# Kernel tuning notes

Measured on AMD Instinct MI355X. Metric: run time of the kernel, lower is better.

## Reference

```python
import jax, jax.numpy as jnp
import numpy as np

B, N, K, CLS = 256, 15, 520, 800  # batch, points per streamline, k+k_global, classes
EPS = 1e-5


def _bn(x, g, b, m, v, axis=1):
    # eval-mode BatchNorm with running stats
    shape = [1] * x.ndim
    shape[axis] = -1
    rs = lambda a: a.reshape(shape)
    return rs(g) * (x - rs(m)) * jax.lax.rsqrt(rs(v) + EPS) + rs(b)


def setup_inputs():
    key = jax.random.key(0)
    kit = iter(jax.random.split(key, 24))
    nk = lambda: next(kit)
    p = {}
    p["pts"] = jax.random.normal(nk(), (B, N, 3), jnp.float32)
    p["label"] = jax.random.randint(nk(), (B,), 0, CLS)
    p["info_point_set"] = jax.random.normal(nk(), (B, K, N, 3), jnp.float32)

    def lin(cout, cin):
        w = jax.random.normal(nk(), (cout, cin), jnp.float32) * (1.0 / np.sqrt(cin))
        return w, jnp.zeros((cout,), jnp.float32)

    def bn(c):
        return (jnp.ones((c,), jnp.float32), jnp.zeros((c,), jnp.float32),
                jax.random.normal(nk(), (c,), jnp.float32) * 0.05,
                jnp.ones((c,), jnp.float32))

    p["w_info"], p["b_info"] = lin(64, 6)
    p["g_info"], p["be_info"], p["m_info"], p["v_info"] = bn(64)
    p["w2"], p["b2"] = lin(128, 64)
    p["g2"], p["be2"], p["m2"], p["v2"] = bn(128)
    p["w3"], p["b3"] = lin(1024, 128)
    p["g3"], p["be3"], p["m3"], p["v3"] = bn(1024)
    p["wf1"], p["bf1"] = lin(512, 1024)
    p["gf1"], p["bef1"], p["mf1"], p["vf1"] = bn(512)
    p["wf2"], p["bf2"] = lin(256, 512)
    p["gf2"], p["bef2"], p["mf2"], p["vf2"] = bn(256)
    p["wf3"], p["bf3"] = lin(CLS, 256)
    return p


def reference(pts, label, info_point_set,
              w_info, b_info, g_info, be_info, m_info, v_info,
              w2, b2, g2, be2, m2, v2,
              w3, b3, g3, be3, m3, v3,
              wf1, bf1, gf1, bef1, mf1, vf1,
              wf2, bf2, gf2, bef2, mf2, vf2,
              wf3, bf3):
    x = jnp.transpose(pts, (0, 2, 1))                      # [B,3,N]
    ips = jnp.transpose(info_point_set, (0, 3, 2, 1))      # [B,3,N,K]
    xr = jnp.broadcast_to(x[..., None], ips.shape)         # [B,3,N,K]
    h = jnp.concatenate([ips - xr, xr], axis=1)            # [B,6,N,K]
    h = jnp.einsum('oc,bcnk->bonk', w_info, h) + b_info[None, :, None, None]
    h = jax.nn.relu(_bn(h, g_info, be_info, m_info, v_info))
    h = jnp.max(h, axis=-1)                                # [B,64,N]  (max over neighbors)
    h2 = jax.nn.relu(_bn(jnp.einsum('oc,bcn->bon', w2, h) + b2[None, :, None],
                         g2, be2, m2, v2))                 # [B,128,N]
    h3 = _bn(jnp.einsum('oc,bcn->bon', w3, h2) + b3[None, :, None],
             g3, be3, m3, v3)                              # [B,1024,N]
    g = jnp.max(h3, axis=2)                                # [B,1024] global max-pool
    f1 = jax.nn.relu(_bn(g @ wf1.T + bf1, gf1, bef1, mf1, vf1, axis=1))
    f2 = jax.nn.relu(_bn(f1 @ wf2.T + bf2, gf2, bef2, mf2, vf2, axis=1))  # dropout identity (eval)
    ret = f2 @ wf3.T + bf3                                 # [B,CLS]
    return (ret, f2)
```

## Files before the change

kernel.cpp:

```cpp
#include <hip/hip_runtime.h>
#include <math.h>

#define EPS 1e-5f

typedef __attribute__((ext_vector_type(8))) short short8v;
typedef __attribute__((ext_vector_type(4))) float f32x4;
typedef __attribute__((ext_vector_type(16))) float f32x16;

__device__ __forceinline__ unsigned short bf16r(float x) {
    unsigned u = __float_as_uint(x);
    return (unsigned short)((u + 0x7FFFu + ((u >> 16) & 1u)) >> 16);
}
__device__ __forceinline__ float bf2f(unsigned short h) {
    return __uint_as_float(((unsigned)h) << 16);
}
__device__ __forceinline__ unsigned packhl(float x) {
    const unsigned short h = bf16r(x);
    const unsigned short l = bf16r(x - bf2f(h));
    return (unsigned)h | ((unsigned)l << 16);
}

__global__ __launch_bounds__(256) void k_pre(
    const float* __restrict__ w3, const float* __restrict__ b3,
    const float* __restrict__ g3, const float* __restrict__ be3,
    const float* __restrict__ m3, const float* __restrict__ v3,
    const float* __restrict__ w2, const float* __restrict__ b2,
    const float* __restrict__ g2, const float* __restrict__ be2,
    const float* __restrict__ m2, const float* __restrict__ v2,
    const float* __restrict__ w_info, const float* __restrict__ b_info,
    const float* __restrict__ g_info, const float* __restrict__ be_info,
    const float* __restrict__ m_info, const float* __restrict__ v_info,
    const float* __restrict__ bf1, const float* __restrict__ gf1,
    const float* __restrict__ bef1, const float* __restrict__ mf1,
    const float* __restrict__ vf1,
    const float* __restrict__ bf2, const float* __restrict__ gf2,
    const float* __restrict__ bef2, const float* __restrict__ mf2,
    const float* __restrict__ vf2,
    const float* __restrict__ wf1, const float* __restrict__ wf2,
    const float* __restrict__ wf3,
    unsigned short* __restrict__ Bh, unsigned short* __restrict__ Bl,
    float* __restrict__ bias3,
    float4* __restrict__ w2q, float* __restrict__ bias2,
    unsigned short* __restrict__ Bedge,
    float4* __restrict__ qTab4,
    float* __restrict__ sf1, float* __restrict__ cf1,
    float* __restrict__ sf2, float* __restrict__ cf2,
    unsigned short* __restrict__ B1h, unsigned short* __restrict__ B1l,
    unsigned short* __restrict__ B2h, unsigned short* __restrict__ B2l,
    unsigned short* __restrict__ B3h, unsigned short* __restrict__ B3l)
{
    const int blk = blockIdx.x, tid = threadIdx.x;
    if (blk < 64) {
        const int t = blk * 256 + tid;
        const int kt = t >> 12;
        const int nt = (t >> 6) & 63;
        const int lane = t & 63;
        const int o  = nt * 16 + (lane & 15);
        const int kb = kt * 32 + ((lane >> 4) << 3);
        const float a3 = g3[o] * rsqrtf(v3[o] + EPS);
        #pragma unroll
        for (int j = 0; j < 8; ++j) {
            const float wv = a3 * w3[(size_t)o * 128 + kb + j];
            const unsigned short hi = bf16r(wv);
            Bh[(size_t)t * 8 + j] = hi;
            Bl[(size_t)t * 8 + j] = bf16r(wv - bf2f(hi));
        }
    } else if (blk == 64) {
        for (int idx = tid; idx < 2048; idx += 256) {
            const int o2 = idx & 127, cq = idx >> 7;
            const float a2 = g2[o2] * rsqrtf(v2[o2] + EPS);
            const float4 w = *(const float4*)(w2 + (size_t)o2 * 64 + cq * 4);
            w2q[cq * 128 + o2] = make_float4(a2 * w.x, a2 * w.y, a2 * w.z, a2 * w.w);
        }
        if (tid < 128) {
            const float a2 = g2[tid] * rsqrtf(v2[tid] + EPS);
            bias2[tid] = a2 * (b2[tid] - m2[tid]) + be2[tid];
        }
    } else if (blk == 65) {
        if (tid < 128) {
            const int nt = tid >> 6, lane = tid & 63;
            const int grp = lane >> 5;
            const int o = nt * 32 + (lane & 31);
            const float a = g_info[o] * rsqrtf(v_info[o] + EPS);
            const float c0 = a * w_info[o*6+0];
            const float c1 = a * w_info[o*6+1];
            const float c2 = a * w_info[o*6+2];
            const unsigned short ch0 = bf16r(c0), ch1 = bf16r(c1), ch2 = bf16r(c2);
            const unsigned short cl0 = bf16r(c0 - bf2f(ch0));
            const unsigned short cl1 = bf16r(c1 - bf2f(ch1));
            const unsigned short cl2 = bf16r(c2 - bf2f(ch2));
            unsigned short out[8] = {0,0,0,0,0,0,0,0};
            if (grp == 0) {
                out[0]=ch0; out[1]=ch1; out[2]=ch2;
                out[3]=cl0; out[4]=cl1; out[5]=cl2;
                out[6]=ch0; out[7]=ch1;
            } else {
                out[0]=ch2;
            }
            #pragma unroll
            for (int j = 0; j < 8; ++j)
                Bedge[(size_t)(nt*64 + lane)*8 + j] = out[j];
        }
        if (tid < 64) {
            const int o = tid;
            const float w0 = w_info[o*6+0], w1 = w_info[o*6+1], w2c = w_info[o*6+2];
            const float w3c = w_info[o*6+3], w4 = w_info[o*6+4], w5 = w_info[o*6+5];
            const float a = g_info[o] * rsqrtf(v_info[o] + EPS);
            qTab4[o] = make_float4(a*(w3c-w0), a*(w4-w1), a*(w5-w2c),
                                   a*(b_info[o]-m_info[o]) + be_info[o]);
        }
        for (int c = tid; c < 1024; c += 256) {
            const float a3 = g3[c] * rsqrtf(v3[c] + EPS);
            bias3[c] = a3 * (b3[c] - m3[c]) + be3[c];
        }
        for (int c = tid; c < 512; c += 256) {
            const float s = gf1[c] * rsqrtf(vf1[c] + EPS);
            sf1[c] = s;
            cf1[c] = s * (bf1[c] - mf1[c]) + bef1[c];
        }
        {
            const int c = tid;
            const float s = gf2[c] * rsqrtf(vf2[c] + EPS);
            sf2[c] = s;
            cf2[c] = s * (bf2[c] - mf2[c]) + bef2[c];
        }
    } else if (blk < 322) {
        const int idx = (blk - 66) * 256 + tid;
        const int lane = idx & 63;
        const int nt = (idx >> 6) & 15;
        const int kt = idx >> 10;
        const int n  = nt * 32 + (lane & 31);
        const int kb = kt * 16 + ((lane >> 5) << 3);
        #pragma unroll
        for (int j = 0; j < 8; ++j) {
            const float wv = wf1[(size_t)n * 1024 + kb + j];
            const unsigned short hi = bf16r(wv);
            B1h[(size_t)idx * 8 + j] = hi;
            B1l[(size_t)idx * 8 + j] = bf16r(wv - bf2f(hi));
        }
    } else if (blk < 386) {
        const int idx = (blk - 322) * 256 + tid;
        const int lane = idx & 63;
        const int nt = (idx >> 6) & 7;
        const int kt = idx >> 9;
        const int n  = nt * 32 + (lane & 31);
        const int kb = kt * 16 + ((lane >> 5) << 3);
        #pragma unroll
        for (int j = 0; j < 8; ++j) {
            const float wv = wf2[(size_t)n * 512 + kb + j];
            const unsigned short hi = bf16r(wv);
            B2h[(size_t)idx * 8 + j] = hi;
            B2l[(size_t)idx * 8 + j] = bf16r(wv - bf2f(hi));
        }
    } else {
        const int idx = (blk - 386) * 256 + tid;
        const int lane = idx & 63;
        const int g6 = idx >> 6;
        const int nt = g6 % 25;
        const int kt = g6 / 25;
        const int n  = nt * 32 + (lane & 31);
        const int kb = kt * 16 + ((lane >> 5) << 3);
        #pragma unroll
        for (int j = 0; j < 8; ++j) {
            const float wv = wf3[(size_t)n * 256 + kb + j];
            const unsigned short hi = bf16r(wv);
            B3h[(size_t)idx * 8 + j] = hi;
            B3l[(size_t)idx * 8 + j] = bf16r(wv - bf2f(hi));
        }
    }
}

__global__ __launch_bounds__(512) void k_edgeS3(
    const float* __restrict__ pts,
    const float* __restrict__ info,
    const unsigned short* __restrict__ Bedge,
    const float4* __restrict__ qTab4,
    const float4* __restrict__ w2q,
    const float* __restrict__ bias2,
    const unsigned short* __restrict__ Bh,
    const unsigned short* __restrict__ Bl,
    const float* __restrict__ bias3,
    unsigned short* __restrict__ ghi,
    unsigned short* __restrict__ glo)
{
    __shared__ unsigned dsb[23400];
    __shared__ float h1s[960];
    __shared__ unsigned short h2hL[2048];
    __shared__ unsigned short h2lL[2048];

    const int tid = threadIdx.x;
    const int b = blockIdx.x;

    {
        const float4* src = (const float4*)(info + (size_t)b * 23400);
        uint4* dst = (uint4*)dsb;
        for (int i = tid; i < 5850; i += 512) {
            const float4 v = src[i];
            uint4 pv;
            pv.x = packhl(v.x); pv.y = packhl(v.y);
            pv.z = packhl(v.z); pv.w = packhl(v.w);
            dst[i] = pv;
        }
    }
    __syncthreads();

    const int wave = tid >> 6, lane = tid & 63;
    const int la = lane & 31;
    const bool hiHalf = lane >= 32;

    {
        short8v bfrag0 = *(const short8v*)(Bedge + (size_t)(0*64 + lane)*8);
        short8v bfrag1 = *(const short8v*)(Bedge + (size_t)(1*64 + lane)*8);

        const f32x16 zero16 = {0.f,0.f,0.f,0.f,0.f,0.f,0.f,0.f,
                               0.f,0.f,0.f,0.f,0.f,0.f,0.f,0.f};

        for (int n = wave; n < 15; n += 8) {
            float m0 = -INFINITY, m1 = -INFINITY;
            const unsigned* pb = dsb + n*3;

            unsigned w0 = 0, w1 = 0, w2 = 0;
            {
                const unsigned* p = pb + la*45;
                if (!hiHalf) { w0 = p[0]; w1 = p[1]; }
                w2 = p[2];
            }

            #pragma unroll 1
            for (int mt = 0; mt < 17; ++mt) {
                unsigned nw0 = 0, nw1 = 0, nw2 = 0;
                if (mt < 16) {
                    int nrow = (mt+1)*32 + la;
                    nrow = nrow > 519 ? 519 : nrow;
                    const unsigned* p = pb + nrow*45;
                    if (!hiHalf) { nw0 = p[0]; nw1 = p[1]; }
                    nw2 = p[2];
                }
                int4 ai;
                if (!hiHalf) {
                    ai.x = (int)((w0 & 0xFFFFu) | (w1 << 16));
                    ai.y = (int)((w2 & 0xFFFFu) | (w0 << 16));
                    ai.z = (int)((w1 & 0xFFFFu) | (w2 << 16));
                    ai.w = (int)((w0 >> 16) | (w1 & 0xFFFF0000u));
                } else {
                    ai.x = (int)(w2 >> 16);
                    ai.y = 0; ai.z = 0; ai.w = 0;
                }
                const short8v afrag = *(short8v*)&ai;
                const f32x16 r0 = __builtin_amdgcn_mfma_f32_32x32x16_bf16(afrag, bfrag0, zero16, 0,0,0);
                const f32x16 r1 = __builtin_amdgcn_mfma_f32_32x32x16_bf16(afrag, bfrag1, zero16, 0,0,0);
                #pragma unroll
                for (int c = 0; c < 16; c += 4) {
                    m0 = fmaxf(m0, fmaxf(fmaxf(r0[c], r0[c+1]),
                                         fmaxf(r0[c+2], r0[c+3])));
                    m1 = fmaxf(m1, fmaxf(fmaxf(r1[c], r1[c+1]),
                                         fmaxf(r1[c+2], r1[c+3])));
                }
                w0 = nw0; w1 = nw1; w2 = nw2;
            }
            m0 = fmaxf(m0, __shfl_xor(m0, 32));
            m1 = fmaxf(m1, __shfl_xor(m1, 32));

            if (lane < 32) {
                const float x0 = pts[b*45 + n*3 + 0];
                const float x1 = pts[b*45 + n*3 + 1];
                const float x2 = pts[b*45 + n*3 + 2];
                {
                    const int o = lane;
                    const float4 qv = qTab4[o];
                    const float bias = fmaf(qv.x, x0, fmaf(qv.y, x1, fmaf(qv.z, x2, qv.w)));
                    h1s[n*64 + o] = fmaxf(m0 + bias, 0.f);
                }
                {
                    const int o = 32 + lane;
                    const float4 qv = qTab4[o];
                    const float bias = fmaf(qv.x, x0, fmaf(qv.y, x1, fmaf(qv.z, x2, qv.w)));
                    h1s[n*64 + o] = fmaxf(m1 + bias, 0.f);
                }
            }
        }
    }
    __syncthreads();

    for (int idx = tid; idx < 2048; idx += 512) {
        const int o2 = idx & 127, n = idx >> 7;
        float val = 0.f;
        if (n < 15) {
            float acc = 0.f;
            #pragma unroll
            for (int cq = 0; cq < 16; ++cq) {
                const float4 h4 = *(const float4*)(&h1s[n*64 + cq*4]);
                const float4 w4 = w2q[cq*128 + o2];
                acc = fmaf(w4.x, h4.x, fmaf(w4.y, h4.y,
                      fmaf(w4.z, h4.z, fmaf(w4.w, h4.w, acc))));
            }
            val = fmaxf(acc + bias2[o2], 0.f);
        }
        const unsigned short hi = bf16r(val);
        const unsigned short lo = bf16r(val - bf2f(hi));
        h2hL[idx] = hi;
        h2lL[idx] = lo;
    }
    __syncthreads();

    {
        const int arow = lane & 15, agrp = lane >> 4;

        short8v ahi[4], alo[4];
        {
            const unsigned short* Ab = h2hL + arow*128 + agrp*8;
            const unsigned short* Al = h2lL + arow*128 + agrp*8;
            #pragma unroll
            for (int kt = 0; kt < 4; ++kt) {
                ahi[kt] = *(const short8v*)(Ab + kt*32);
                alo[kt] = *(const short8v*)(Al + kt*32);
            }
        }

        for (int ntl = 0; ntl < 8; ++ntl) {
            const int nt = wave * 8 + ntl;
            f32x4 a0 = {0.f, 0.f, 0.f, 0.f};
            f32x4 a1 = a0, a2 = a0;
            #pragma unroll
            for (int kt = 0; kt < 4; ++kt) {
                const size_t off = (((size_t)kt*64 + nt)*64 + lane) * 8;
                const short8v bh = *(const short8v*)(Bh + off);
                const short8v bl = *(const short8v*)(Bl + off);
                a0 = __builtin_amdgcn_mfma_f32_16x16x32_bf16(ahi[kt], bh, a0, 0, 0, 0);
                a1 = __builtin_amdgcn_mfma_f32_16x16x32_bf16(ahi[kt], bl, a1, 0, 0, 0);
                a2 = __builtin_amdgcn_mfma_f32_16x16x32_bf16(alo[kt], bh, a2, 0, 0, 0);
            }
            const float r0 = a0[0] + a1[0] + a2[0];
            const float r1 = a0[1] + a1[1] + a2[1];
            const float r2 = a0[2] + a1[2] + a2[2];
            const float r3 = a0[3] + a1[3] + a2[3];
            float m = fmaxf(fmaxf(r0, r1), r2);
            if (agrp != 3) m = fmaxf(m, r3);
            m = fmaxf(m, __shfl_xor(m, 16));
            m = fmaxf(m, __shfl_xor(m, 32));
            if (lane < 16) {
                const float val = m + bias3[nt*16 + lane];
                const unsigned short hi = bf16r(val);
                ghi[(size_t)b*1024 + nt*16 + lane] = hi;
                glo[(size_t)b*1024 + nt*16 + lane] = bf16r(val - bf2f(hi));
            }
        }
    }
}

__global__ __launch_bounds__(256) void k_fc1m(
    const unsigned short* __restrict__ gh,
    const unsigned short* __restrict__ gl,
    const unsigned short* __restrict__ B1h,
    const unsigned short* __restrict__ B1l,
    const float* __restrict__ sf1, const float* __restrict__ cf1,
    unsigned short* __restrict__ f1h,
    unsigned short* __restrict__ f1l)
{
    __shared__ float part[4][32][33];

    const int tid = threadIdx.x;
    const int bm = blockIdx.x * 32, bn = blockIdx.y * 32;
    const int wave = tid >> 6, lane = tid & 63;
    const int m = bm + (lane & 31);
    const int kgrp = (lane >> 5) << 3;

    f32x16 acc = {0.f,0.f,0.f,0.f,0.f,0.f,0.f,0.f,
                  0.f,0.f,0.f,0.f,0.f,0.f,0.f,0.f};

    for (int kt = wave*16; kt < wave*16 + 16; ++kt) {
        const int kb = kt*16 + kgrp;
        const short8v ah = *(const short8v*)(gh + (size_t)m*1024 + kb);
        const short8v al = *(const short8v*)(gl + (size_t)m*1024 + kb);
        const size_t boff = ((size_t)kt*1024 + blockIdx.y*64 + lane) * 8;
        const short8v bh = *(const short8v*)(B1h + boff);
        const short8v bl = *(const short8v*)(B1l + boff);
        acc = __builtin_amdgcn_mfma_f32_32x32x16_bf16(ah, bh, acc, 0,0,0);
        acc = __builtin_amdgcn_mfma_f32_32x32x16_bf16(ah, bl, acc, 0,0,0);
        acc = __builtin_amdgcn_mfma_f32_32x32x16_bf16(al, bh, acc, 0,0,0);
    }
    {
        const int n = lane & 31, mhl = (lane >> 5) << 2;
        #pragma unroll
        for (int reg = 0; reg < 16; ++reg) {
            const int mrow = (reg & 3) + 8*(reg >> 2) + mhl;
            part[wave][mrow][n] = acc[reg];
        }
    }
    __syncthreads();

    for (int i = tid; i < 1024; i += 256) {
        const int lm = i >> 5, ln = i & 31;
        const float sum = part[0][lm][ln] + part[1][lm][ln]
                        + part[2][lm][ln] + part[3][lm][ln];
        const int ch = bn + ln;
        const float val = fmaxf(fmaf(sf1[ch], sum, cf1[ch]), 0.f);
        const unsigned short hi = bf16r(val);
        f1h[(size_t)(bm + lm)*512 + ch] = hi;
        f1l[(size_t)(bm + lm)*512 + ch] = bf16r(val - bf2f(hi));
    }
}

__global__ __launch_bounds__(256) void k_fc2m(
    const unsigned short* __restrict__ f1h,
    const unsigned short* __restrict__ f1l,
    const unsigned short* __restrict__ B2h,
    const unsigned short* __restrict__ B2l,
    const float* __restrict__ sf2, const float* __restrict__ cf2,
    float* __restrict__ f2out,
    unsigned short* __restrict__ f2h,
    unsigned short* __restrict__ f2l)
{
    __shared__ float part[4][32][33];

    const int tid = threadIdx.x;
    const int bm = blockIdx.x * 32, bn = blockIdx.y * 32;
    const int wave = tid >> 6, lane = tid & 63;
    const int m = bm + (lane & 31);
    const int kgrp = (lane >> 5) << 3;

    f32x16 acc = {0.f,0.f,0.f,0.f,0.f,0.f,0.f,0.f,
                  0.f,0.f,0.f,0.f,0.f,0.f,0.f,0.f};

    for (int kt = wave*8; kt < wave*8 + 8; ++kt) {
        const int kb = kt*16 + kgrp;
        const short8v ah = *(const short8v*)(f1h + (size_t)m*512 + kb);
        const short8v al = *(const short8v*)(f1l + (size_t)m*512 + kb);
        const size_t boff = ((size_t)kt*512 + blockIdx.y*64 + lane) * 8;
        const short8v bh = *(const short8v*)(B2h + boff);
        const short8v bl = *(const short8v*)(B2l + boff);
        acc = __builtin_amdgcn_mfma_f32_32x32x16_bf16(ah, bh, acc, 0,0,0);
        acc = __builtin_amdgcn_mfma_f32_32x32x16_bf16(ah, bl, acc, 0,0,0);
        acc = __builtin_amdgcn_mfma_f32_32x32x16_bf16(al, bh, acc, 0,0,0);
    }
    {
        const int n = lane & 31, mhl = (lane >> 5) << 2;
        #pragma unroll
        for (int reg = 0; reg < 16; ++reg) {
            const int mrow = (reg & 3) + 8*(reg >> 2) + mhl;
            part[wave][mrow][n] = acc[reg];
        }
    }
    __syncthreads();

    for (int i = tid; i < 1024; i += 256) {
        const int lm = i >> 5, ln = i & 31;
        const float sum = part[0][lm][ln] + part[1][lm][ln]
                        + part[2][lm][ln] + part[3][lm][ln];
        const int ch = bn + ln;
        const float val = fmaxf(fmaf(sf2[ch], sum, cf2[ch]), 0.f);
        const size_t o = (size_t)(bm + lm)*256 + ch;
        f2out[o] = val;
        const unsigned short hi = bf16r(val);
        f2h[o] = hi;
        f2l[o] = bf16r(val - bf2f(hi));
    }
}

__global__ __launch_bounds__(256) void k_fc3m(
    const unsigned short* __restrict__ f2h,
    const unsigned short* __restrict__ f2l,
    const unsigned short* __restrict__ B3h,
    const unsigned short* __restrict__ B3l,
    const float* __restrict__ bias,
    float* __restrict__ C)
{
    __shared__ float part[4][32][33];

    const int tid = threadIdx.x;
    const int bm = blockIdx.x * 32;
    const int wave = tid >> 6, lane = tid & 63;
    const int m = bm + (lane & 31);
    const int kgrp = (lane >> 5) << 3;

    f32x16 acc = {0.f,0.f,0.f,0.f,0.f,0.f,0.f,0.f,
                  0.f,0.f,0.f,0.f,0.f,0.f,0.f,0.f};

    for (int kt = wave*4; kt < wave*4 + 4; ++kt) {
        const int kb = kt*16 + kgrp;
        const short8v ah = *(const short8v*)(f2h + (size_t)m*256 + kb);
        const short8v al = *(const short8v*)(f2l + (size_t)m*256 + kb);
        const size_t boff = (((size_t)kt*25 + blockIdx.y)*64 + lane) * 8;
        const short8v bh = *(const short8v*)(B3h + boff);
        const short8v bl = *(const short8v*)(B3l + boff);
        acc = __builtin_amdgcn_mfma_f32_32x32x16_bf16(ah, bh, acc, 0,0,0);
        acc = __builtin_amdgcn_mfma_f32_32x32x16_bf16(ah, bl, acc, 0,0,0);
        acc = __builtin_amdgcn_mfma_f32_32x32x16_bf16(al, bh, acc, 0,0,0);
    }
    {
        const int n = lane & 31, mhl = (lane >> 5) << 2;
        #pragma unroll
        for (int reg = 0; reg < 16; ++reg) {
            const int mrow = (reg & 3) + 8*(reg >> 2) + mhl;
            part[wave][mrow][n] = acc[reg];
        }
    }
    __syncthreads();

    for (int i = tid; i < 1024; i += 256) {
        const int lm = i >> 5, ln = i & 31;
        const float sum = part[0][lm][ln] + part[1][lm][ln]
                        + part[2][lm][ln] + part[3][lm][ln];
        const int ch = blockIdx.y * 32 + ln;
        C[(size_t)(bm + lm)*800 + ch] = sum + bias[ch];
    }
}

extern "C" void kernel_launch(void* const* d_in, const int* in_sizes, int n_in,
                              void* d_out, int out_size, void* d_ws, size_t ws_size,
                              hipStream_t stream)
{
    const float* pts     = (const float*)d_in[0];
    const float* info    = (const float*)d_in[2];
    const float* w_info  = (const float*)d_in[3];
    const float* b_info  = (const float*)d_in[4];
    const float* g_info  = (const float*)d_in[5];
    const float* be_info = (const float*)d_in[6];
    const float* m_info  = (const float*)d_in[7];
    const float* v_info  = (const float*)d_in[8];
    const float* w2      = (const float*)d_in[9];
    const float* b2      = (const float*)d_in[10];
    const float* g2      = (const float*)d_in[11];
    const float* be2     = (const float*)d_in[12];
    const float* m2      = (const float*)d_in[13];
    const float* v2      = (const float*)d_in[14];
    const float* w3      = (const float*)d_in[15];
    const float* b3      = (const float*)d_in[16];
    const float* g3      = (const float*)d_in[17];
    const float* be3     = (const float*)d_in[18];
    const float* m3      = (const float*)d_in[19];
    const float* v3      = (const float*)d_in[20];
    const float* wf1     = (const float*)d_in[21];
    const float* bf1     = (const float*)d_in[22];
    const float* gf1     = (const float*)d_in[23];
    const float* bef1    = (const float*)d_in[24];
    const float* mf1     = (const float*)d_in[25];
    const float* vf1     = (const float*)d_in[26];
    const float* wf2     = (const float*)d_in[27];
    const float* bf2     = (const float*)d_in[28];
    const float* gf2     = (const float*)d_in[29];
    const float* bef2    = (const float*)d_in[30];
    const float* mf2     = (const float*)d_in[31];
    const float* vf2     = (const float*)d_in[32];
    const float* wf3     = (const float*)d_in[33];
    const float* bf3     = (const float*)d_in[34];

    float* ws = (float*)d_ws;
    unsigned short* ghi   = (unsigned short*)(ws + 0);
    unsigned short* glo   = (unsigned short*)(ws + 131072);
    unsigned short* f2h   = (unsigned short*)(ws + 0);
    unsigned short* f2l   = (unsigned short*)(ws + 32768);
    unsigned short* f1h   = (unsigned short*)(ws + 262144);
    unsigned short* f1l   = (unsigned short*)(ws + 327680);
    unsigned short* B1h   = (unsigned short*)(ws + 393216);
    unsigned short* B1l   = (unsigned short*)(ws + 655360);
    unsigned short* B2h   = (unsigned short*)(ws + 917504);
    unsigned short* B2l   = (unsigned short*)(ws + 983040);
    unsigned short* B3h   = (unsigned short*)(ws + 1048576);
    unsigned short* B3l   = (unsigned short*)(ws + 1150976);
    unsigned short* Bh    = (unsigned short*)(ws + 1277952);
    unsigned short* Bl    = (unsigned short*)(ws + 1343488);
    float*          bias3 = ws + 1409024;
    float4*         w2q   = (float4*)(ws + 1410048);
    float*          bias2 = ws + 1418240;
    float4*         qTab4 = (float4*)(ws + 1418624);
    float*          sf1   = ws + 1418880;
    float*          cf1   = ws + 1419392;
    float*          sf2   = ws + 1419904;
    float*          cf2   = ws + 1420160;
    unsigned short* Bedge = (unsigned short*)(ws + 1420416);

    float* ret = (float*)d_out;
    float* f2  = ret + 256 * 800;

    k_pre<<<486, 256, 0, stream>>>(
        w3, b3, g3, be3, m3, v3,
        w2, b2, g2, be2, m2, v2,
        w_info, b_info, g_info, be_info, m_info, v_info,
        bf1, gf1, bef1, mf1, vf1,
        bf2, gf2, bef2, mf2, vf2,
        wf1, wf2, wf3,
        Bh, Bl, bias3, w2q, bias2, Bedge, qTab4, sf1, cf1, sf2, cf2,
        B1h, B1l, B2h, B2l, B3h, B3l);

    k_edgeS3<<<256, 512, 0, stream>>>(pts, info, Bedge, qTab4,
                                      w2q, bias2, Bh, Bl, bias3, ghi, glo);

    k_fc1m<<<dim3(8, 16), 256, 0, stream>>>(ghi, glo, B1h, B1l,
                                            sf1, cf1, f1h, f1l);

    k_fc2m<<<dim3(8, 8), 256, 0, stream>>>(f1h, f1l, B2h, B2l,
                                           sf2, cf2, f2, f2h, f2l);

    k_fc3m<<<dim3(8, 25), 256, 0, stream>>>(f2h, f2l, B3h, B3l, bf3, ret);
}
```

Measured before the change: 60.16 us.

## Stage edge-conv input in two halves to halve shared memory footprint

The per-batch neighbor tile is now loaded and packed into LDS in two halves of 260 neighbors each instead of all 520 at once. The edge MFMA/max loop runs over each half, carrying running maxima across halves. This roughly halves LDS usage (from ~94KB to ~47KB for dsb), which could let two blocks share a CU and overlap loads with compute. The cost is an extra barrier and a serialized load phase per half.

```diff
diff --git a/kernel.cpp b/kernel.cpp
--- a/kernel.cpp
+++ b/kernel.cpp
@@ -18,6 +18,51 @@
     const unsigned short h = bf16r(x);
     const unsigned short l = bf16r(x - bf2f(h));
     return (unsigned)h | ((unsigned)l << 16);
+}
+
+__device__ __forceinline__ void edge_accum(
+    const unsigned* __restrict__ dsb, int n, int la, bool hiHalf,
+    short8v bfrag0, short8v bfrag1, float& m0, float& m1)
+{
+    const f32x16 zero16 = {0.f,0.f,0.f,0.f,0.f,0.f,0.f,0.f,
+                           0.f,0.f,0.f,0.f,0.f,0.f,0.f,0.f};
+    const unsigned* pb = dsb + n*3;
+    unsigned w0 = 0, w1 = 0, w2 = 0;
+    {
+        const unsigned* p = pb + la*45;
+        if (!hiHalf) { w0 = p[0]; w1 = p[1]; }
+        w2 = p[2];
+    }
+    #pragma unroll 1
+    for (int mt = 0; mt < 9; ++mt) {
+        unsigned nw0 = 0, nw1 = 0, nw2 = 0;
+        if (mt < 8) {
+            int nrow = (mt+1)*32 + la;
+            nrow = nrow > 259 ? 259 : nrow;
+            const unsigned* p = pb + nrow*45;
+            if (!hiHalf) { nw0 = p[0]; nw1 = p[1]; }
+            nw2 = p[2];
+        }
+        int4 ai;
+        if (!hiHalf) {
+            ai.x = (int)((w0 & 0xFFFFu) | (w1 << 16));
+            ai.y = (int)((w2 & 0xFFFFu) | (w0 << 16));
+            ai.z = (int)((w1 & 0xFFFFu) | (w2 << 16));
+            ai.w = (int)((w0 >> 16) | (w1 & 0xFFFF0000u));
+        } else {
+            ai.x = (int)(w2 >> 16);
+            ai.y = 0; ai.z = 0; ai.w = 0;
+        }
+        const short8v afrag = *(short8v*)&ai;
+        const f32x16 r0 = __builtin_amdgcn_mfma_f32_32x32x16_bf16(afrag, bfrag0, zero16, 0,0,0);
+        const f32x16 r1 = __builtin_amdgcn_mfma_f32_32x32x16_bf16(afrag, bfrag1, zero16, 0,0,0);
+        #pragma unroll
+        for (int c = 0; c < 16; c += 4) {
+            m0 = fmaxf(m0, fmaxf(fmaxf(r0[c], r0[c+1]), fmaxf(r0[c+2], r0[c+3])));
+            m1 = fmaxf(m1, fmaxf(fmaxf(r1[c], r1[c+1]), fmaxf(r1[c+2], r1[c+3])));
+        }
+        w0 = nw0; w1 = nw1; w2 = nw2;
+    }
 }
 
 __global__ __launch_bounds__(256) void k_pre(
@@ -183,7 +228,7 @@
     unsigned short* __restrict__ ghi,
     unsigned short* __restrict__ glo)
 {
-    __shared__ unsigned dsb[23400];
+    __shared__ unsigned dsb[11700];
     __shared__ float h1s[960];
     __shared__ unsigned short h2hL[2048];
     __shared__ unsigned short h2lL[2048];
@@ -191,91 +236,75 @@
     const int tid = threadIdx.x;
     const int b = blockIdx.x;
 
-    {
-        const float4* src = (const float4*)(info + (size_t)b * 23400);
-        uint4* dst = (uint4*)dsb;
-        for (int i = tid; i < 5850; i += 512) {
-            const float4 v = src[i];
-            uint4 pv;
-            pv.x = packhl(v.x); pv.y = packhl(v.y);
-            pv.z = packhl(v.z); pv.w = packhl(v.w);
-            dst[i] = pv;
-        }
-    }
-    __syncthreads();
-
     const int wave = tid >> 6, lane = tid & 63;
     const int la = lane & 31;
     const bool hiHalf = lane >= 32;
 
+    const short8v bfrag0 = *(const short8v*)(Bedge + (size_t)(0*64 + lane)*8);
+    const short8v bfrag1 = *(const short8v*)(Bedge + (size_t)(1*64 + lane)*8);
+
+    const int n0 = wave;
+    const int n1 = wave + 8;
+    float m0a = -INFINITY, m1a = -INFINITY;
+    float m0b = -INFINITY, m1b = -INFINITY;
+
+    #pragma unroll 1
+    for (int half = 0; half < 2; ++half) {
+        if (half) __syncthreads();
+        {
+            const float4* src = (const float4*)(info + (size_t)b * 23400 + half * 11700);
+            uint4* dst = (uint4*)dsb;
+            for (int i = tid; i < 2925; i += 512) {
+                const float4 v = src[i];
+                uint4 pv;
+                pv.x = packhl(v.x); pv.y = packhl(v.y);
+                pv.z = packhl(v.z); pv.w = packhl(v.w);
+                dst[i] = pv;
+            }
+        }
+        __syncthreads();
+
+        edge_accum(dsb, n0, la, hiHalf, bfrag0, bfrag1, m0a, m1a);
+        if (n1 < 15)
+            edge_accum(dsb, n1, la, hiHalf, bfrag0, bfrag1, m0b, m1b);
+    }
+
     {
-        short8v bfrag0 = *(const short8v*)(Bedge + (size_t)(0*64 + lane)*8);
-        short8v bfrag1 = *(const short8v*)(Bedge + (size_t)(1*64 + lane)*8);
-
-        const f32x16 zero16 = {0.f,0.f,0.f,0.f,0.f,0.f,0.f,0.f,
-                               0.f,0.f,0.f,0.f,0.f,0.f,0.f,0.f};
-
-        for (int n = wave; n < 15; n += 8) {
-            float m0 = -INFINITY, m1 = -INFINITY;
-            const unsigned* pb = dsb + n*3;
-
-            unsigned w0 = 0, w1 = 0, w2 = 0;
+        m0a = fmaxf(m0a, __shfl_xor(m0a, 32));
+        m1a = fmaxf(m1a, __shfl_xor(m1a, 32));
+        m0b = fmaxf(m0b, __shfl_xor(m0b, 32));
+        m1b = fmaxf(m1b, __shfl_xor(m1b, 32));
+        if (lane < 32) {
             {
-                const unsigned* p = pb + la*45;
-                if (!hiHalf) { w0 = p[0]; w1 = p[1]; }
-                w2 = p[2];
-            }
-
-            #pragma unroll 1
-            for (int mt = 0; mt < 17; ++mt) {
-                unsigned nw0 = 0, nw1 = 0, nw2 = 0;
-                if (mt < 16) {
-                    int nrow = (mt+1)*32 + la;
-                    nrow = nrow > 519 ? 519 : nrow;
-                    const unsigned* p = pb + nrow*45;
-                    if (!hiHalf) { nw0 = p[0]; nw1 = p[1]; }
-                    nw2 = p[2];
-                }
-                int4 ai;
-                if (!hiHalf) {
-                    ai.x = (int)((w0 & 0xFFFFu) | (w1 << 16));
-                    ai.y = (int)((w2 & 0xFFFFu) | (w0 << 16));
-                    ai.z = (int)((w1 & 0xFFFFu) | (w2 << 16));
-                    ai.w = (int)((w0 >> 16) | (w1 & 0xFFFF0000u));
-                } else {
-                    ai.x = (int)(w2 >> 16);
-                    ai.y = 0; ai.z = 0; ai.w = 0;
-                }
-                const short8v afrag = *(short8v*)&ai;
-                const f32x16 r0 = __builtin_amdgcn_mfma_f32_32x32x16_bf16(afrag, bfrag0, zero16, 0,0,0);
-                const f32x16 r1 = __builtin_amdgcn_mfma_f32_32x32x16_bf16(afrag, bfrag1, zero16, 0,0,0);
-                #pragma unroll
-                for (int c = 0; c < 16; c += 4) {
-                    m0 = fmaxf(m0, fmaxf(fmaxf(r0[c], r0[c+1]),
-                                         fmaxf(r0[c+2], r0[c+3])));
-                    m1 = fmaxf(m1, fmaxf(fmaxf(r1[c], r1[c+1]),
-                                         fmaxf(r1[c+2], r1[c+3])));
-                }
-                w0 = nw0; w1 = nw1; w2 = nw2;
-            }
-            m0 = fmaxf(m0, __shfl_xor(m0, 32));
-            m1 = fmaxf(m1, __shfl_xor(m1, 32));
-
-            if (lane < 32) {
+                const int n = n0;
                 const float x0 = pts[b*45 + n*3 + 0];
                 const float x1 = pts[b*45 + n*3 + 1];
                 const float x2 = pts[b*45 + n*3 + 2];
                 {
-                    const int o = lane;
-                    const float4 qv = qTab4[o];
+                    const float4 qv = qTab4[lane];
                     const float bias = fmaf(qv.x, x0, fmaf(qv.y, x1, fmaf(qv.z, x2, qv.w)));
-                    h1s[n*64 + o] = fmaxf(m0 + bias, 0.f);
+                    h1s[n*64 + lane] = fmaxf(m0a + bias, 0.f);
                 }
                 {
-                    const int o = 32 + lane;
-                    const float4 qv = qTab4[o];
+                    const float4 qv = qTab4[32 + lane];
                     const float bias = fmaf(qv.x, x0, fmaf(qv.y, x1, fmaf(qv.z, x2, qv.w)));
-                    h1s[n*64 + o] = fmaxf(m1 + bias, 0.f);
+                    h1s[n*64 + 32 + lane] = fmaxf(m1a + bias, 0.f);
+                }
+            }
+            if (n1 < 15) {
+                const int n = n1;
+                const float x0 = pts[b*45 + n*3 + 0];
+                const float x1 = pts[b*45 + n*3 + 1];
+                const float x2 = pts[b*45 + n*3 + 2];
+                {
+                    const float4 qv = qTab4[lane];
+                    const float bias = fmaf(qv.x, x0, fmaf(qv.y, x1, fmaf(qv.z, x2, qv.w)));
+                    h1s[n*64 + lane] = fmaxf(m0b + bias, 0.f);
+                }
+                {
+                    const float4 qv = qTab4[32 + lane];
+                    const float bias = fmaf(qv.x, x0, fmaf(qv.y, x1, fmaf(qv.z, x2, qv.w)));
+                    h1s[n*64 + 32 + lane] = fmaxf(m1b + bias, 0.f);
                 }
             }
         }
```

Result: slower. 65.95 us (+9.6%).
